# Optimization experiments

Hardware: AMD Instinct MI355X
Metric: run time of the kernel (lower is better)

Reference implementation:

```python
import jax, jax.numpy as jnp
import numpy as np
from math import sqrt

D = 64
HEADS = 8
SEQ = 4096


def setup_inputs() -> dict:
    key = jax.random.key(0)
    ks = jax.random.split(key, 11)
    d, h = D, HEADS
    scale = 1.0 / sqrt(d)
    inp = {
        "q": jax.random.normal(ks[0], (SEQ, d), dtype=jnp.float32),
        "k": jax.random.normal(ks[1], (SEQ, d), dtype=jnp.float32),
        "v": jax.random.normal(ks[2], (SEQ, d), dtype=jnp.float32),
        # Linear(d, d*heads) weights stored as [in, out]; biases [out]
        "qw_w": jax.random.normal(ks[3], (d, d * h), dtype=jnp.float32) * scale,
        "qw_b": jax.random.normal(ks[4], (d * h,), dtype=jnp.float32) * 0.01,
        "kw_w": jax.random.normal(ks[5], (d, d * h), dtype=jnp.float32) * scale,
        "kw_b": jax.random.normal(ks[6], (d * h,), dtype=jnp.float32) * 0.01,
        "vw_w": jax.random.normal(ks[7], (d, d * h), dtype=jnp.float32) * scale,
        "vw_b": jax.random.normal(ks[8], (d * h,), dtype=jnp.float32) * 0.01,
        "ow_w": jax.random.normal(ks[9], (d * h, d), dtype=jnp.float32) * (1.0 / sqrt(d * h)),
        "ow_b": jax.random.normal(ks[10], (d,), dtype=jnp.float32) * 0.01,
    }
    return inp


def reference(q, k, v, qw_w, qw_b, kw_w, kw_b, vw_w, vw_b, ow_w, ow_b):
    d, h = D, HEADS
    # Project: [S, d] @ [d, d*h] -> [S, d*h], then raw reshape to [h, S, d]
    # (matches torch .view(heads, -1, d) on the contiguous projection)
    qh = (q @ qw_w + qw_b).reshape(h, -1, d)
    kh = (k @ kw_w + kw_b).reshape(h, -1, d)
    vh = (v @ vw_w + vw_b).reshape(h, -1, d)
    # scores: [h, S, S]
    scores = jnp.einsum("hqd,hkd->hqk", qh, kh) / sqrt(d)
    attn = jax.nn.softmax(scores, axis=-1)
    ctx = jnp.einsum("hqk,hkd->hqd", attn, vh)  # [h, S, d]
    ctx = ctx.reshape(-1, h * d)  # row-major reshape, matches torch .reshape
    return ctx @ ow_w + ow_b  # [S, d]
```

## Files before the change

### kernel.cpp

```cpp
#include <hip/hip_runtime.h>
#include <stdint.h>

#define SEQL 4096
#define NHEAD 8
#define DHEAD 64
#define HEADELEMS (SEQL * DHEAD)
#define KVBLK 64
#define TPH 32

typedef unsigned short u16;
typedef __bf16 bf16x8 __attribute__((ext_vector_type(8)));
typedef float f32x16 __attribute__((ext_vector_type(16)));

extern "C" __device__ float __ocml_native_exp2_f32(float);

__device__ __forceinline__ u16 f2bf(float f) {
  union { float f; uint32_t u; } x; x.f = f;
  uint32_t r = x.u + 0x7fffu + ((x.u >> 16) & 1u);
  return (u16)(r >> 16);
}

__device__ __forceinline__ uint32_t cvt_pk_bf16(float lo, float hi) {
  uint32_t r;
  asm("v_cvt_pk_bf16_f32 %0, %1, %2" : "=v"(r) : "v"(lo), "v"(hi));
  return r;
}

__device__ __forceinline__ void pl32_swap(uint32_t& dst, uint32_t& src) {
  asm("v_permlane32_swap_b32 %0, %1" : "+v"(dst), "+v"(src));
}

#define GLDS16(g, l)                                                            \
  __builtin_amdgcn_global_load_lds(                                             \
      (const __attribute__((address_space(1))) uint32_t*)(g),                   \
      (__attribute__((address_space(3))) uint32_t*)(l), 16, 0, 0)

__global__ __launch_bounds__(256) void proj_kernel(
    const float* __restrict__ q, const float* __restrict__ k, const float* __restrict__ v,
    const float* __restrict__ qw, const float* __restrict__ qb,
    const float* __restrict__ kw, const float* __restrict__ kb,
    const float* __restrict__ vw, const float* __restrict__ vb,
    u16* __restrict__ Qp, u16* __restrict__ Kp, u16* __restrict__ vhT) {
  const float* X; const float* W; const float* B; float scale;
  if (blockIdx.y == 0)      { X = q; W = qw; B = qb; scale = 0.125f * 1.44269504089f; }
  else if (blockIdx.y == 1) { X = k; W = kw; B = kb; scale = 1.0f; }
  else                      { X = v; W = vw; B = vb; scale = 1.0f; }

  __shared__ float xs[16][64];
  __shared__ __align__(16) u16 vtile[64][136];
  const int t = threadIdx.x;
  const int rowbase = blockIdx.x * 16;
  for (int i = t; i < 16 * 64; i += 256) xs[i >> 6][i & 63] = X[rowbase * 64 + i];
  __syncthreads();

  const int c0 = t * 2;
  float acc0[16] = {}, acc1[16] = {};
  for (int kk = 0; kk < 64; ++kk) {
    const float2 w = *(const float2*)(W + kk * 512 + c0);
    #pragma unroll
    for (int r = 0; r < 16; ++r) {
      const float x = xs[r][kk];
      acc0[r] = fmaf(x, w.x, acc0[r]);
      acc1[r] = fmaf(x, w.y, acc1[r]);
    }
  }
  const float b0 = B[c0], b1 = B[c0 + 1];

  if (blockIdx.y != 2) {
    u16* __restrict__ P = (blockIdx.y == 0) ? Qp : Kp;
    #pragma unroll
    for (int r = 0; r < 16; ++r) {
      const u16 o0 = f2bf((acc0[r] + b0) * scale);
      const u16 o1 = f2bf((acc1[r] + b1) * scale);
      *(uint32_t*)(P + (rowbase + r) * 512 + c0) = ((uint32_t)o1 << 16) | (uint32_t)o0;
    }
  } else {
    const int dd = c0 & 63, cg = c0 >> 6;
    #pragma unroll
    for (int r = 0; r < 16; ++r) {
      vtile[dd][r * 8 + cg]     = f2bf(acc0[r] + b0);
      vtile[dd + 1][r * 8 + cg] = f2bf(acc1[r] + b1);
    }
    __syncthreads();
    const int h = rowbase >> 9;
    const int ibase = (rowbase & 511) * 8;
    u16* __restrict__ dst = vhT + h * HEADELEMS;
    #pragma unroll
    for (int rep = 0; rep < 4; ++rep) {
      const int n = t + rep * 256;
      const int d2 = n >> 4, m = n & 15;
      *(uint4*)(dst + d2 * 4096 + ibase + m * 8) = *(const uint4*)(&vtile[d2][m * 8]);
    }
  }
}

__global__ __launch_bounds__(256, 2) void attn_kernel(
    const u16* __restrict__ Qp, const u16* __restrict__ Kp,
    const u16* __restrict__ vhT, float* __restrict__ cxp, float* __restrict__ lsp) {
  const int h = blockIdx.x & 7, idx = blockIdx.x >> 3;
  const int qb = idx >> 1, half = idx & 1;
  const int t = threadIdx.x, lane = t & 63;
  const int l32 = lane & 31, hi = lane >> 5;

  __shared__ __align__(16) char smem[5 * 16384];

  const u16* __restrict__ Qh = Qp + h * HEADELEMS;
  const u16* __restrict__ Kh = Kp + h * HEADELEMS;
  const u16* __restrict__ VTh = vhT + h * HEADELEMS;

  int koff[2], voff[2];
  #pragma unroll
  for (int i = 0; i < 2; ++i) {
    const int n = t + i * 256;
    const int r = n >> 3, c = (n & 7) ^ (r & 7);
    koff[i] = r * 64 + c * 8;
    voff[i] = r * 4096 + c * 8;
  }
  const int wuni = (t & 192) * 16;
  char* const qlds = smem + 65536;

#define STAGE(j, slot)                                                         \
  {                                                                            \
    const int kb_ = (half * TPH + (j)) * KVBLK;                                \
    GLDS16(Kh + kb_ * 64 + koff[0], (slot));                                   \
    GLDS16(Kh + kb_ * 64 + koff[1], (slot) + 4096);                            \
    GLDS16(VTh + kb_ + voff[0], (slot) + 8192);                                \
    GLDS16(VTh + kb_ + voff[1], (slot) + 12288);                               \
  }

  {
    const u16* __restrict__ qsrc = Qh + qb * 128 * 64;
    #pragma unroll
    for (int i = 0; i < 4; ++i) {
      const int n = t + i * 256;
      GLDS16(qsrc + (n >> 3) * 64 + (n & 7) * 8, qlds + i * 4096 + wuni);
    }
  }
  __builtin_amdgcn_sched_barrier(0);
  STAGE(0, smem + wuni);
  __builtin_amdgcn_sched_barrier(0);
  STAGE(1, smem + 16384 + wuni);
  __builtin_amdgcn_sched_barrier(0);
  STAGE(2, smem + 32768 + wuni);
  __builtin_amdgcn_sched_barrier(0);

  asm volatile("s_waitcnt vmcnt(12)" ::: "memory");
  __builtin_amdgcn_s_barrier();
  __builtin_amdgcn_sched_barrier(0);

  const int qrl = (t >> 6) * 32 + l32;
  bf16x8 qf[4];
  #pragma unroll
  for (int ks = 0; ks < 4; ++ks)
    qf[ks] = *(const bf16x8*)(qlds + qrl * 128 + ks * 32 + hi * 16);

  const f32x16 z16 = {0,0,0,0,0,0,0,0,0,0,0,0,0,0,0,0};
  f32x16 ca0 = z16, ca1 = z16;
  float ls[4] = {0.f, 0.f, 0.f, 0.f};

  for (int it = 0; it < TPH; ++it) {
    if (it < TPH - 2)       asm volatile("s_waitcnt vmcnt(8) lgkmcnt(0)" ::: "memory");
    else if (it == TPH - 2) asm volatile("s_waitcnt vmcnt(4) lgkmcnt(0)" ::: "memory");
    else                    asm volatile("s_waitcnt vmcnt(0) lgkmcnt(0)" ::: "memory");
    __builtin_amdgcn_s_barrier();
    __builtin_amdgcn_sched_barrier(0);

    char* const cb = smem + (it & 3) * 16384;
    if (it + 3 < TPH) STAGE(it + 3, smem + ((it + 3) & 3) * 16384 + wuni);
    __builtin_amdgcn_sched_barrier(0);

    f32x16 s0 = z16, s1 = z16;
    const int ar0 = l32, ar1 = l32 + 32;
    __builtin_amdgcn_s_setprio(1);
    #pragma unroll
    for (int ks = 0; ks < 4; ++ks) {
      const int c = ks * 2 + hi;
      const bf16x8 k0 = *(const bf16x8*)(cb + ar0 * 128 + ((c ^ (ar0 & 7)) * 16));
      const bf16x8 k1 = *(const bf16x8*)(cb + ar1 * 128 + ((c ^ (ar1 & 7)) * 16));
      s0 = __builtin_amdgcn_mfma_f32_32x32x16_bf16(k0, qf[ks], s0, 0, 0, 0);
      s1 = __builtin_amdgcn_mfma_f32_32x32x16_bf16(k1, qf[ks], s1, 0, 0, 0);
    }
    __builtin_amdgcn_s_setprio(0);

    float e[32];
    #pragma unroll
    for (int r = 0; r < 16; ++r) { e[r] = __ocml_native_exp2_f32(s0[r]); ls[r & 3] += e[r]; }
    #pragma unroll
    for (int r = 0; r < 16; ++r) { e[16 + r] = __ocml_native_exp2_f32(s1[r]); ls[r & 3] += e[16 + r]; }

    #pragma unroll
    for (int ksl = 0; ksl < 4; ++ksl) {
      uint32_t w0 = cvt_pk_bf16(e[ksl * 8 + 0], e[ksl * 8 + 1]);
      uint32_t w1 = cvt_pk_bf16(e[ksl * 8 + 2], e[ksl * 8 + 3]);
      uint32_t w2 = cvt_pk_bf16(e[ksl * 8 + 4], e[ksl * 8 + 5]);
      uint32_t w3 = cvt_pk_bf16(e[ksl * 8 + 6], e[ksl * 8 + 7]);
      pl32_swap(w0, w2);
      pl32_swap(w1, w3);
      union { uint32_t u[4]; bf16x8 v; } pw;
      pw.u[0] = w0; pw.u[1] = w1; pw.u[2] = w2; pw.u[3] = w3;
      const bf16x8 paf = pw.v;

      const int cl = ksl * 2 + hi;
      const int vr0 = l32, vr1 = l32 + 32;
      const bf16x8 v0 = *(const bf16x8*)(cb + 8192 + vr0 * 128 + ((cl ^ (vr0 & 7)) * 16));
      const bf16x8 v1 = *(const bf16x8*)(cb + 8192 + vr1 * 128 + ((cl ^ (vr1 & 7)) * 16));
      __builtin_amdgcn_s_setprio(1);
      ca0 = __builtin_amdgcn_mfma_f32_32x32x16_bf16(paf, v0, ca0, 0, 0, 0);
      ca1 = __builtin_amdgcn_mfma_f32_32x32x16_bf16(paf, v1, ca1, 0, 0, 0);
      __builtin_amdgcn_s_setprio(0);
    }
  }
#undef STAGE

  float lsum = (ls[0] + ls[1]) + (ls[2] + ls[3]);
  lsum += __shfl_xor(lsum, 32);
  const int q0 = qb * 128 + (t >> 6) * 32;
  float* __restrict__ ch = cxp + (half * NHEAD + h) * HEADELEMS;
  #pragma unroll
  for (int reg = 0; reg < 16; ++reg) {
    const int crw = (reg & 3) + 8 * (reg >> 2) + 4 * hi;
    ch[(q0 + crw) * 64 + l32]      = ca0[reg];
    ch[(q0 + crw) * 64 + 32 + l32] = ca1[reg];
  }
  if (hi == 0) lsp[(half * NHEAD + h) * SEQL + q0 + l32] = lsum;
}

__global__ __launch_bounds__(256) void outproj_kernel(
    const float* __restrict__ cxp, const float* __restrict__ lsp,
    const float* __restrict__ W, const float* __restrict__ B,
    float* __restrict__ out) {
  const int t = threadIdx.x;
  const int r0 = blockIdx.x * 8;
  const int hh = r0 >> 9;
  const int sb0 = (r0 & 511) * 8;

  __shared__ float cn[64][64];
  __shared__ float invs[64];

  if (t < 64)
    invs[t] = 1.0f / (lsp[hh * SEQL + sb0 + t] + lsp[(NHEAD + hh) * SEQL + sb0 + t]);
  __syncthreads();

  const float* __restrict__ a0 = cxp + hh * HEADELEMS + sb0 * 64;
  const float* __restrict__ b0 = cxp + (NHEAD + hh) * HEADELEMS + sb0 * 64;
  #pragma unroll
  for (int i = 0; i < 4; ++i) {
    const int n = (t + i * 256) * 4;
    const int s = n >> 6;
    const float4 av = *(const float4*)(a0 + n);
    const float4 bv = *(const float4*)(b0 + n);
    const float inv = invs[s];
    float4 cv;
    cv.x = (av.x + bv.x) * inv; cv.y = (av.y + bv.y) * inv;
    cv.z = (av.z + bv.z) * inv; cv.w = (av.w + bv.w) * inv;
    *(float4*)(&cn[s][n & 63]) = cv;
  }
  __syncthreads();

  const int col = t & 63;
  const int lr = (t >> 6) * 2;
  float acc0 = 0.f, acc1 = 0.f;
  #pragma unroll 8
  for (int kk = 0; kk < 512; ++kk) {
    const float wv = W[kk * 64 + col];
    acc0 = fmaf(cn[lr * 8 + (kk >> 6)][kk & 63], wv, acc0);
    acc1 = fmaf(cn[lr * 8 + 8 + (kk >> 6)][kk & 63], wv, acc1);
  }
  const float b = B[col];
  out[(r0 + lr) * 64 + col] = acc0 + b;
  out[(r0 + lr + 1) * 64 + col] = acc1 + b;
}

extern "C" void kernel_launch(void* const* d_in, const int* in_sizes, int n_in,
                              void* d_out, int out_size, void* d_ws, size_t ws_size,
                              hipStream_t stream) {
  const float* q  = (const float*)d_in[0];
  const float* k  = (const float*)d_in[1];
  const float* v  = (const float*)d_in[2];
  const float* qw = (const float*)d_in[3];
  const float* qb = (const float*)d_in[4];
  const float* kw = (const float*)d_in[5];
  const float* kb = (const float*)d_in[6];
  const float* vw = (const float*)d_in[7];
  const float* vb = (const float*)d_in[8];
  const float* ow = (const float*)d_in[9];
  const float* ob = (const float*)d_in[10];

  char* ws = (char*)d_ws;
  u16* Qp    = (u16*)(ws);
  u16* Kp    = (u16*)(ws + (4u << 20));
  u16* vhT   = (u16*)(ws + (8u << 20));
  float* cxp = (float*)(ws + (12u << 20));
  float* lsp = (float*)(ws + (28u << 20));
  float* out = (float*)d_out;

  proj_kernel<<<dim3(SEQL / 16, 3), 256, 0, stream>>>(q, k, v, qw, qb, kw, kb, vw, vb,
                                                      Qp, Kp, vhT);
  attn_kernel<<<512, 256, 0, stream>>>(Qp, Kp, vhT, cxp, lsp);
  outproj_kernel<<<SEQL / 8, 256, 0, stream>>>(cxp, lsp, ow, ob, out);
}
```

Before: 91.67 us.

## Double Q rows per attention block and split KV four ways

Each attention block now handles 256 query rows, two 32-row Q fragments per wave, so every K/V tile loaded into LDS feeds twice as many MFMAs. To keep the grid at 512 blocks, the KV range is split into 4 parts (SPLIT template) instead of 2. The LDS pipeline shrinks from 4 stages to 3 to make room for the larger Q tile. The out-projection sums the 4 partial contexts and row sums, which adds global traffic and register pressure, and falls back to SPLIT=2 if the workspace is too small.

```diff
diff --git a/kernel.cpp b/kernel.cpp
--- a/kernel.cpp
+++ b/kernel.cpp
@@ -6,7 +6,6 @@
 #define DHEAD 64
 #define HEADELEMS (SEQL * DHEAD)
 #define KVBLK 64
-#define TPH 32
 
 typedef unsigned short u16;
 typedef __bf16 bf16x8 __attribute__((ext_vector_type(8)));
@@ -28,6 +27,18 @@
 
 __device__ __forceinline__ void pl32_swap(uint32_t& dst, uint32_t& src) {
   asm("v_permlane32_swap_b32 %0, %1" : "+v"(dst), "+v"(src));
+}
+
+__device__ __forceinline__ bf16x8 pack_paf(const float* e8) {
+  uint32_t w0 = cvt_pk_bf16(e8[0], e8[1]);
+  uint32_t w1 = cvt_pk_bf16(e8[2], e8[3]);
+  uint32_t w2 = cvt_pk_bf16(e8[4], e8[5]);
+  uint32_t w3 = cvt_pk_bf16(e8[6], e8[7]);
+  pl32_swap(w0, w2);
+  pl32_swap(w1, w3);
+  union { uint32_t u[4]; bf16x8 v; } pw;
+  pw.u[0] = w0; pw.u[1] = w1; pw.u[2] = w2; pw.u[3] = w3;
+  return pw.v;
 }
 
 #define GLDS16(g, l)                                                            \
@@ -94,15 +105,18 @@
   }
 }
 
+template <int SPLIT>
 __global__ __launch_bounds__(256, 2) void attn_kernel(
     const u16* __restrict__ Qp, const u16* __restrict__ Kp,
     const u16* __restrict__ vhT, float* __restrict__ cxp, float* __restrict__ lsp) {
+  constexpr int TPQ = 64 / SPLIT;
   const int h = blockIdx.x & 7, idx = blockIdx.x >> 3;
-  const int qb = idx >> 1, half = idx & 1;
+  const int qb = idx / SPLIT, part = idx % SPLIT;
   const int t = threadIdx.x, lane = t & 63;
   const int l32 = lane & 31, hi = lane >> 5;
 
-  __shared__ __align__(16) char smem[5 * 16384];
+  __shared__ __align__(16) char smem[3 * 16384 + 32768];
+  char* const qlds = smem + 49152;
 
   const u16* __restrict__ Qh = Qp + h * HEADELEMS;
   const u16* __restrict__ Kh = Kp + h * HEADELEMS;
@@ -117,11 +131,10 @@
     voff[i] = r * 4096 + c * 8;
   }
   const int wuni = (t & 192) * 16;
-  char* const qlds = smem + 65536;
 
 #define STAGE(j, slot)                                                         \
   {                                                                            \
-    const int kb_ = (half * TPH + (j)) * KVBLK;                                \
+    const int kb_ = (part * TPQ + (j)) * KVBLK;                                \
     GLDS16(Kh + kb_ * 64 + koff[0], (slot));                                   \
     GLDS16(Kh + kb_ * 64 + koff[1], (slot) + 4096);                            \
     GLDS16(VTh + kb_ + voff[0], (slot) + 8192);                                \
@@ -129,9 +142,9 @@
   }
 
   {
-    const u16* __restrict__ qsrc = Qh + qb * 128 * 64;
-    #pragma unroll
-    for (int i = 0; i < 4; ++i) {
+    const u16* __restrict__ qsrc = Qh + qb * 256 * 64;
+    #pragma unroll
+    for (int i = 0; i < 8; ++i) {
       const int n = t + i * 256;
       GLDS16(qsrc + (n >> 3) * 64 + (n & 7) * 8, qlds + i * 4096 + wuni);
     }
@@ -141,35 +154,34 @@
   __builtin_amdgcn_sched_barrier(0);
   STAGE(1, smem + 16384 + wuni);
   __builtin_amdgcn_sched_barrier(0);
-  STAGE(2, smem + 32768 + wuni);
-  __builtin_amdgcn_sched_barrier(0);
-
-  asm volatile("s_waitcnt vmcnt(12)" ::: "memory");
+
+  asm volatile("s_waitcnt vmcnt(8)" ::: "memory");
   __builtin_amdgcn_s_barrier();
   __builtin_amdgcn_sched_barrier(0);
 
-  const int qrl = (t >> 6) * 32 + l32;
-  bf16x8 qf[4];
+  const int qrlA = (t >> 6) * 64 + l32;
+  bf16x8 qfA[4], qfB[4];
   #pragma unroll
-  for (int ks = 0; ks < 4; ++ks)
-    qf[ks] = *(const bf16x8*)(qlds + qrl * 128 + ks * 32 + hi * 16);
+  for (int ks = 0; ks < 4; ++ks) {
+    qfA[ks] = *(const bf16x8*)(qlds + qrlA * 128 + ks * 32 + hi * 16);
+    qfB[ks] = *(const bf16x8*)(qlds + (qrlA + 32) * 128 + ks * 32 + hi * 16);
+  }
 
   const f32x16 z16 = {0,0,0,0,0,0,0,0,0,0,0,0,0,0,0,0};
-  f32x16 ca0 = z16, ca1 = z16;
-  float ls[4] = {0.f, 0.f, 0.f, 0.f};
-
-  for (int it = 0; it < TPH; ++it) {
-    if (it < TPH - 2)       asm volatile("s_waitcnt vmcnt(8) lgkmcnt(0)" ::: "memory");
-    else if (it == TPH - 2) asm volatile("s_waitcnt vmcnt(4) lgkmcnt(0)" ::: "memory");
-    else                    asm volatile("s_waitcnt vmcnt(0) lgkmcnt(0)" ::: "memory");
+  f32x16 caA0 = z16, caA1 = z16, caB0 = z16, caB1 = z16;
+  float lsA[4] = {0.f, 0.f, 0.f, 0.f}, lsB[4] = {0.f, 0.f, 0.f, 0.f};
+
+  for (int it = 0; it < TPQ; ++it) {
+    if (it < TPQ - 1) asm volatile("s_waitcnt vmcnt(4) lgkmcnt(0)" ::: "memory");
+    else              asm volatile("s_waitcnt vmcnt(0) lgkmcnt(0)" ::: "memory");
     __builtin_amdgcn_s_barrier();
     __builtin_amdgcn_sched_barrier(0);
 
-    char* const cb = smem + (it & 3) * 16384;
-    if (it + 3 < TPH) STAGE(it + 3, smem + ((it + 3) & 3) * 16384 + wuni);
+    char* const cb = smem + (it % 3) * 16384;
+    if (it + 2 < TPQ) STAGE(it + 2, smem + ((it + 2) % 3) * 16384 + wuni);
     __builtin_amdgcn_sched_barrier(0);
 
-    f32x16 s0 = z16, s1 = z16;
+    f32x16 sA0 = z16, sA1 = z16, sB0 = z16, sB1 = z16;
     const int ar0 = l32, ar1 = l32 + 32;
     __builtin_amdgcn_s_setprio(1);
     #pragma unroll
@@ -177,54 +189,70 @@
       const int c = ks * 2 + hi;
       const bf16x8 k0 = *(const bf16x8*)(cb + ar0 * 128 + ((c ^ (ar0 & 7)) * 16));
       const bf16x8 k1 = *(const bf16x8*)(cb + ar1 * 128 + ((c ^ (ar1 & 7)) * 16));
-      s0 = __builtin_amdgcn_mfma_f32_32x32x16_bf16(k0, qf[ks], s0, 0, 0, 0);
-      s1 = __builtin_amdgcn_mfma_f32_32x32x16_bf16(k1, qf[ks], s1, 0, 0, 0);
+      sA0 = __builtin_amdgcn_mfma_f32_32x32x16_bf16(k0, qfA[ks], sA0, 0, 0, 0);
+      sA1 = __builtin_amdgcn_mfma_f32_32x32x16_bf16(k1, qfA[ks], sA1, 0, 0, 0);
+      sB0 = __builtin_amdgcn_mfma_f32_32x32x16_bf16(k0, qfB[ks], sB0, 0, 0, 0);
+      sB1 = __builtin_amdgcn_mfma_f32_32x32x16_bf16(k1, qfB[ks], sB1, 0, 0, 0);
     }
     __builtin_amdgcn_s_setprio(0);
 
-    float e[32];
-    #pragma unroll
-    for (int r = 0; r < 16; ++r) { e[r] = __ocml_native_exp2_f32(s0[r]); ls[r & 3] += e[r]; }
-    #pragma unroll
-    for (int r = 0; r < 16; ++r) { e[16 + r] = __ocml_native_exp2_f32(s1[r]); ls[r & 3] += e[16 + r]; }
+    bf16x8 pafA[4], pafB[4];
+    {
+      float e[32];
+      #pragma unroll
+      for (int r = 0; r < 16; ++r) { e[r] = __ocml_native_exp2_f32(sA0[r]); lsA[r & 3] += e[r]; }
+      #pragma unroll
+      for (int r = 0; r < 16; ++r) { e[16 + r] = __ocml_native_exp2_f32(sA1[r]); lsA[r & 3] += e[16 + r]; }
+      #pragma unroll
+      for (int ksl = 0; ksl < 4; ++ksl) pafA[ksl] = pack_paf(e + ksl * 8);
+    }
+    {
+      float e[32];
+      #pragma unroll
+      for (int r = 0; r < 16; ++r) { e[r] = __ocml_native_exp2_f32(sB0[r]); lsB[r & 3] += e[r]; }
+      #pragma unroll
+      for (int r = 0; r < 16; ++r) { e[16 + r] = __ocml_native_exp2_f32(sB1[r]); lsB[r & 3] += e[16 + r]; }
+      #pragma unroll
+      for (int ksl = 0; ksl < 4; ++ksl) pafB[ksl] = pack_paf(e + ksl * 8);
+    }
 
     #pragma unroll
     for (int ksl = 0; ksl < 4; ++ksl) {
-      uint32_t w0 = cvt_pk_bf16(e[ksl * 8 + 0], e[ksl * 8 + 1]);
-      uint32_t w1 = cvt_pk_bf16(e[ksl * 8 + 2], e[ksl * 8 + 3]);
-      uint32_t w2 = cvt_pk_bf16(e[ksl * 8 + 4], e[ksl * 8 + 5]);
-      uint32_t w3 = cvt_pk_bf16(e[ksl * 8 + 6], e[ksl * 8 + 7]);
-      pl32_swap(w0, w2);
-      pl32_swap(w1, w3);
-      union { uint32_t u[4]; bf16x8 v; } pw;
-      pw.u[0] = w0; pw.u[1] = w1; pw.u[2] = w2; pw.u[3] = w3;
-      const bf16x8 paf = pw.v;
-
       const int cl = ksl * 2 + hi;
       const int vr0 = l32, vr1 = l32 + 32;
       const bf16x8 v0 = *(const bf16x8*)(cb + 8192 + vr0 * 128 + ((cl ^ (vr0 & 7)) * 16));
       const bf16x8 v1 = *(const bf16x8*)(cb + 8192 + vr1 * 128 + ((cl ^ (vr1 & 7)) * 16));
       __builtin_amdgcn_s_setprio(1);
-      ca0 = __builtin_amdgcn_mfma_f32_32x32x16_bf16(paf, v0, ca0, 0, 0, 0);
-      ca1 = __builtin_amdgcn_mfma_f32_32x32x16_bf16(paf, v1, ca1, 0, 0, 0);
+      caA0 = __builtin_amdgcn_mfma_f32_32x32x16_bf16(pafA[ksl], v0, caA0, 0, 0, 0);
+      caA1 = __builtin_amdgcn_mfma_f32_32x32x16_bf16(pafA[ksl], v1, caA1, 0, 0, 0);
+      caB0 = __builtin_amdgcn_mfma_f32_32x32x16_bf16(pafB[ksl], v0, caB0, 0, 0, 0);
+      caB1 = __builtin_amdgcn_mfma_f32_32x32x16_bf16(pafB[ksl], v1, caB1, 0, 0, 0);
       __builtin_amdgcn_s_setprio(0);
     }
   }
 #undef STAGE
 
-  float lsum = (ls[0] + ls[1]) + (ls[2] + ls[3]);
-  lsum += __shfl_xor(lsum, 32);
-  const int q0 = qb * 128 + (t >> 6) * 32;
-  float* __restrict__ ch = cxp + (half * NHEAD + h) * HEADELEMS;
+  float lsumA = (lsA[0] + lsA[1]) + (lsA[2] + lsA[3]);
+  float lsumB = (lsB[0] + lsB[1]) + (lsB[2] + lsB[3]);
+  lsumA += __shfl_xor(lsumA, 32);
+  lsumB += __shfl_xor(lsumB, 32);
+  const int q0 = qb * 256 + (t >> 6) * 64;
+  float* __restrict__ ch = cxp + (part * NHEAD + h) * HEADELEMS;
   #pragma unroll
   for (int reg = 0; reg < 16; ++reg) {
     const int crw = (reg & 3) + 8 * (reg >> 2) + 4 * hi;
-    ch[(q0 + crw) * 64 + l32]      = ca0[reg];
-    ch[(q0 + crw) * 64 + 32 + l32] = ca1[reg];
-  }
-  if (hi == 0) lsp[(half * NHEAD + h) * SEQL + q0 + l32] = lsum;
-}
-
+    ch[(q0 + crw) * 64 + l32]           = caA0[reg];
+    ch[(q0 + crw) * 64 + 32 + l32]      = caA1[reg];
+    ch[(q0 + 32 + crw) * 64 + l32]      = caB0[reg];
+    ch[(q0 + 32 + crw) * 64 + 32 + l32] = caB1[reg];
+  }
+  if (hi == 0) {
+    lsp[(part * NHEAD + h) * SEQL + q0 + l32]      = lsumA;
+    lsp[(part * NHEAD + h) * SEQL + q0 + 32 + l32] = lsumB;
+  }
+}
+
+template <int SPLIT>
 __global__ __launch_bounds__(256) void outproj_kernel(
     const float* __restrict__ cxp, const float* __restrict__ lsp,
     const float* __restrict__ W, const float* __restrict__ B,
@@ -237,23 +265,28 @@
   __shared__ float cn[64][64];
   __shared__ float invs[64];
 
-  if (t < 64)
-    invs[t] = 1.0f / (lsp[hh * SEQL + sb0 + t] + lsp[(NHEAD + hh) * SEQL + sb0 + t]);
+  if (t < 64) {
+    float s = 0.f;
+    #pragma unroll
+    for (int p = 0; p < SPLIT; ++p) s += lsp[(p * NHEAD + hh) * SEQL + sb0 + t];
+    invs[t] = 1.0f / s;
+  }
   __syncthreads();
 
-  const float* __restrict__ a0 = cxp + hh * HEADELEMS + sb0 * 64;
-  const float* __restrict__ b0 = cxp + (NHEAD + hh) * HEADELEMS + sb0 * 64;
   #pragma unroll
   for (int i = 0; i < 4; ++i) {
     const int n = (t + i * 256) * 4;
     const int s = n >> 6;
-    const float4 av = *(const float4*)(a0 + n);
-    const float4 bv = *(const float4*)(b0 + n);
+    const int base = hh * HEADELEMS + sb0 * 64 + n;
+    float4 av = *(const float4*)(cxp + base);
+    #pragma unroll
+    for (int p = 1; p < SPLIT; ++p) {
+      const float4 bv = *(const float4*)(cxp + p * NHEAD * HEADELEMS + base);
+      av.x += bv.x; av.y += bv.y; av.z += bv.z; av.w += bv.w;
+    }
     const float inv = invs[s];
-    float4 cv;
-    cv.x = (av.x + bv.x) * inv; cv.y = (av.y + bv.y) * inv;
-    cv.z = (av.z + bv.z) * inv; cv.w = (av.w + bv.w) * inv;
-    *(float4*)(&cn[s][n & 63]) = cv;
+    av.x *= inv; av.y *= inv; av.z *= inv; av.w *= inv;
+    *(float4*)(&cn[s][n & 63]) = av;
   }
   __syncthreads();
 
@@ -291,11 +324,19 @@
   u16* Kp    = (u16*)(ws + (4u << 20));
   u16* vhT   = (u16*)(ws + (8u << 20));
   float* cxp = (float*)(ws + (12u << 20));
-  float* lsp = (float*)(ws + (28u << 20));
   float* out = (float*)d_out;
 
   proj_kernel<<<dim3(SEQL / 16, 3), 256, 0, stream>>>(q, k, v, qw, qb, kw, kb, vw, vb,
                                                       Qp, Kp, vhT);
-  attn_kernel<<<512, 256, 0, stream>>>(Qp, Kp, vhT, cxp, lsp);
-  outproj_kernel<<<SEQL / 8, 256, 0, stream>>>(cxp, lsp, ow, ob, out);
-}
+
+  const size_t need4 = (12u << 20) + 4u * ((8u << 20) + NHEAD * SEQL * 4u);
+  if (ws_size >= need4) {
+    float* lsp = (float*)(ws + (12u << 20) + 4u * (8u << 20));
+    attn_kernel<4><<<16 * 4 * 8, 256, 0, stream>>>(Qp, Kp, vhT, cxp, lsp);
+    outproj_kernel<4><<<SEQL / 8, 256, 0, stream>>>(cxp, lsp, ow, ob, out);
+  } else {
+    float* lsp = (float*)(ws + (12u << 20) + 2u * (8u << 20));
+    attn_kernel<2><<<16 * 2 * 8, 256, 0, stream>>>(Qp, Kp, vhT, cxp, lsp);
+    outproj_kernel<2><<<SEQL / 8, 256, 0, stream>>>(cxp, lsp, ow, ob, out);
+  }
+}
```

Measured after the change: 89.21 us (median of 4 runs). -2.7%, faster.

## Split attention KV range three ways with smaller LDS and higher occupancy

Applied to the files above, without the earlier changes.

Templates the attention kernel on a KV split factor and launches a 3-way split (768 blocks) when workspace allows, falling back to 2. LDS drops from 80KB to 48KB by using a 3-slot ring with prefetch distance 2 and loading Q fragments directly from global instead of staging through LDS. Launch bounds raise to 3 waves/SIMD group for occupancy. The output projection sums SPLIT partial contexts and row sums, which adds partial-buffer traffic, and the shallower prefetch depth may expose more load latency.

```diff
diff --git a/kernel.cpp b/kernel.cpp
--- a/kernel.cpp
+++ b/kernel.cpp
@@ -6,7 +6,6 @@
 #define DHEAD 64
 #define HEADELEMS (SEQL * DHEAD)
 #define KVBLK 64
-#define TPH 32
 
 typedef unsigned short u16;
 typedef __bf16 bf16x8 __attribute__((ext_vector_type(8)));
@@ -28,6 +27,18 @@
 
 __device__ __forceinline__ void pl32_swap(uint32_t& dst, uint32_t& src) {
   asm("v_permlane32_swap_b32 %0, %1" : "+v"(dst), "+v"(src));
+}
+
+__device__ __forceinline__ bf16x8 pack_paf(const float* e8) {
+  uint32_t w0 = cvt_pk_bf16(e8[0], e8[1]);
+  uint32_t w1 = cvt_pk_bf16(e8[2], e8[3]);
+  uint32_t w2 = cvt_pk_bf16(e8[4], e8[5]);
+  uint32_t w3 = cvt_pk_bf16(e8[6], e8[7]);
+  pl32_swap(w0, w2);
+  pl32_swap(w1, w3);
+  union { uint32_t u[4]; bf16x8 v; } pw;
+  pw.u[0] = w0; pw.u[1] = w1; pw.u[2] = w2; pw.u[3] = w3;
+  return pw.v;
 }
 
 #define GLDS16(g, l)                                                            \
@@ -94,15 +105,18 @@
   }
 }
 
-__global__ __launch_bounds__(256, 2) void attn_kernel(
+template <int SPLIT>
+__global__ __launch_bounds__(256, 3) void attn_kernel(
     const u16* __restrict__ Qp, const u16* __restrict__ Kp,
     const u16* __restrict__ vhT, float* __restrict__ cxp, float* __restrict__ lsp) {
   const int h = blockIdx.x & 7, idx = blockIdx.x >> 3;
-  const int qb = idx >> 1, half = idx & 1;
+  const int qb = idx / SPLIT, part = idx % SPLIT;
   const int t = threadIdx.x, lane = t & 63;
   const int l32 = lane & 31, hi = lane >> 5;
-
-  __shared__ __align__(16) char smem[5 * 16384];
+  const int ts = (part * 64) / SPLIT;
+  const int te = ((part + 1) * 64) / SPLIT;
+
+  __shared__ __align__(16) char smem[3 * 16384];
 
   const u16* __restrict__ Qh = Qp + h * HEADELEMS;
   const u16* __restrict__ Kh = Kp + h * HEADELEMS;
@@ -117,56 +131,40 @@
     voff[i] = r * 4096 + c * 8;
   }
   const int wuni = (t & 192) * 16;
-  char* const qlds = smem + 65536;
 
 #define STAGE(j, slot)                                                         \
   {                                                                            \
-    const int kb_ = (half * TPH + (j)) * KVBLK;                                \
+    const int kb_ = (j) * KVBLK;                                               \
     GLDS16(Kh + kb_ * 64 + koff[0], (slot));                                   \
     GLDS16(Kh + kb_ * 64 + koff[1], (slot) + 4096);                            \
     GLDS16(VTh + kb_ + voff[0], (slot) + 8192);                                \
     GLDS16(VTh + kb_ + voff[1], (slot) + 12288);                               \
   }
 
-  {
-    const u16* __restrict__ qsrc = Qh + qb * 128 * 64;
-    #pragma unroll
-    for (int i = 0; i < 4; ++i) {
-      const int n = t + i * 256;
-      GLDS16(qsrc + (n >> 3) * 64 + (n & 7) * 8, qlds + i * 4096 + wuni);
-    }
-  }
-  __builtin_amdgcn_sched_barrier(0);
-  STAGE(0, smem + wuni);
-  __builtin_amdgcn_sched_barrier(0);
-  STAGE(1, smem + 16384 + wuni);
-  __builtin_amdgcn_sched_barrier(0);
-  STAGE(2, smem + 32768 + wuni);
-  __builtin_amdgcn_sched_barrier(0);
-
-  asm volatile("s_waitcnt vmcnt(12)" ::: "memory");
-  __builtin_amdgcn_s_barrier();
-  __builtin_amdgcn_sched_barrier(0);
-
-  const int qrl = (t >> 6) * 32 + l32;
+  const int qrow = qb * 128 + (t >> 6) * 32 + l32;
   bf16x8 qf[4];
   #pragma unroll
   for (int ks = 0; ks < 4; ++ks)
-    qf[ks] = *(const bf16x8*)(qlds + qrl * 128 + ks * 32 + hi * 16);
+    qf[ks] = *(const bf16x8*)(Qh + qrow * 64 + ks * 16 + hi * 8);
+  __builtin_amdgcn_sched_barrier(0);
+
+  STAGE(ts, smem + wuni);
+  __builtin_amdgcn_sched_barrier(0);
+  STAGE(ts + 1, smem + 16384 + wuni);
+  __builtin_amdgcn_sched_barrier(0);
 
   const f32x16 z16 = {0,0,0,0,0,0,0,0,0,0,0,0,0,0,0,0};
   f32x16 ca0 = z16, ca1 = z16;
   float ls[4] = {0.f, 0.f, 0.f, 0.f};
 
-  for (int it = 0; it < TPH; ++it) {
-    if (it < TPH - 2)       asm volatile("s_waitcnt vmcnt(8) lgkmcnt(0)" ::: "memory");
-    else if (it == TPH - 2) asm volatile("s_waitcnt vmcnt(4) lgkmcnt(0)" ::: "memory");
-    else                    asm volatile("s_waitcnt vmcnt(0) lgkmcnt(0)" ::: "memory");
+  for (int it = ts; it < te; ++it) {
+    if (it < te - 1) asm volatile("s_waitcnt vmcnt(4) lgkmcnt(0)" ::: "memory");
+    else             asm volatile("s_waitcnt vmcnt(0) lgkmcnt(0)" ::: "memory");
     __builtin_amdgcn_s_barrier();
     __builtin_amdgcn_sched_barrier(0);
 
-    char* const cb = smem + (it & 3) * 16384;
-    if (it + 3 < TPH) STAGE(it + 3, smem + ((it + 3) & 3) * 16384 + wuni);
+    char* const cb = smem + ((it - ts) % 3) * 16384;
+    if (it + 2 < te) STAGE(it + 2, smem + ((it - ts + 2) % 3) * 16384 + wuni);
     __builtin_amdgcn_sched_barrier(0);
 
     f32x16 s0 = z16, s1 = z16;
@@ -190,16 +188,7 @@
 
     #pragma unroll
     for (int ksl = 0; ksl < 4; ++ksl) {
-      uint32_t w0 = cvt_pk_bf16(e[ksl * 8 + 0], e[ksl * 8 + 1]);
-      uint32_t w1 = cvt_pk_bf16(e[ksl * 8 + 2], e[ksl * 8 + 3]);
-      uint32_t w2 = cvt_pk_bf16(e[ksl * 8 + 4], e[ksl * 8 + 5]);
-      uint32_t w3 = cvt_pk_bf16(e[ksl * 8 + 6], e[ksl * 8 + 7]);
-      pl32_swap(w0, w2);
-      pl32_swap(w1, w3);
-      union { uint32_t u[4]; bf16x8 v; } pw;
-      pw.u[0] = w0; pw.u[1] = w1; pw.u[2] = w2; pw.u[3] = w3;
-      const bf16x8 paf = pw.v;
-
+      const bf16x8 paf = pack_paf(e + ksl * 8);
       const int cl = ksl * 2 + hi;
       const int vr0 = l32, vr1 = l32 + 32;
       const bf16x8 v0 = *(const bf16x8*)(cb + 8192 + vr0 * 128 + ((cl ^ (vr0 & 7)) * 16));
@@ -215,16 +204,17 @@
   float lsum = (ls[0] + ls[1]) + (ls[2] + ls[3]);
   lsum += __shfl_xor(lsum, 32);
   const int q0 = qb * 128 + (t >> 6) * 32;
-  float* __restrict__ ch = cxp + (half * NHEAD + h) * HEADELEMS;
+  float* __restrict__ ch = cxp + (part * NHEAD + h) * HEADELEMS;
   #pragma unroll
   for (int reg = 0; reg < 16; ++reg) {
     const int crw = (reg & 3) + 8 * (reg >> 2) + 4 * hi;
     ch[(q0 + crw) * 64 + l32]      = ca0[reg];
     ch[(q0 + crw) * 64 + 32 + l32] = ca1[reg];
   }
-  if (hi == 0) lsp[(half * NHEAD + h) * SEQL + q0 + l32] = lsum;
-}
-
+  if (hi == 0) lsp[(part * NHEAD + h) * SEQL + q0 + l32] = lsum;
+}
+
+template <int SPLIT>
 __global__ __launch_bounds__(256) void outproj_kernel(
     const float* __restrict__ cxp, const float* __restrict__ lsp,
     const float* __restrict__ W, const float* __restrict__ B,
@@ -237,23 +227,28 @@
   __shared__ float cn[64][64];
   __shared__ float invs[64];
 
-  if (t < 64)
-    invs[t] = 1.0f / (lsp[hh * SEQL + sb0 + t] + lsp[(NHEAD + hh) * SEQL + sb0 + t]);
+  if (t < 64) {
+    float s = 0.f;
+    #pragma unroll
+    for (int p = 0; p < SPLIT; ++p) s += lsp[(p * NHEAD + hh) * SEQL + sb0 + t];
+    invs[t] = 1.0f / s;
+  }
   __syncthreads();
 
-  const float* __restrict__ a0 = cxp + hh * HEADELEMS + sb0 * 64;
-  const float* __restrict__ b0 = cxp + (NHEAD + hh) * HEADELEMS + sb0 * 64;
   #pragma unroll
   for (int i = 0; i < 4; ++i) {
     const int n = (t + i * 256) * 4;
     const int s = n >> 6;
-    const float4 av = *(const float4*)(a0 + n);
-    const float4 bv = *(const float4*)(b0 + n);
+    const int base = hh * HEADELEMS + sb0 * 64 + n;
+    float4 av = *(const float4*)(cxp + base);
+    #pragma unroll
+    for (int p = 1; p < SPLIT; ++p) {
+      const float4 bv = *(const float4*)(cxp + p * NHEAD * HEADELEMS + base);
+      av.x += bv.x; av.y += bv.y; av.z += bv.z; av.w += bv.w;
+    }
     const float inv = invs[s];
-    float4 cv;
-    cv.x = (av.x + bv.x) * inv; cv.y = (av.y + bv.y) * inv;
-    cv.z = (av.z + bv.z) * inv; cv.w = (av.w + bv.w) * inv;
-    *(float4*)(&cn[s][n & 63]) = cv;
+    av.x *= inv; av.y *= inv; av.z *= inv; av.w *= inv;
+    *(float4*)(&cn[s][n & 63]) = av;
   }
   __syncthreads();
 
@@ -291,11 +286,19 @@
   u16* Kp    = (u16*)(ws + (4u << 20));
   u16* vhT   = (u16*)(ws + (8u << 20));
   float* cxp = (float*)(ws + (12u << 20));
-  float* lsp = (float*)(ws + (28u << 20));
   float* out = (float*)d_out;
 
   proj_kernel<<<dim3(SEQL / 16, 3), 256, 0, stream>>>(q, k, v, qw, qb, kw, kb, vw, vb,
                                                       Qp, Kp, vhT);
-  attn_kernel<<<512, 256, 0, stream>>>(Qp, Kp, vhT, cxp, lsp);
-  outproj_kernel<<<SEQL / 8, 256, 0, stream>>>(cxp, lsp, ow, ob, out);
-}
+
+  const size_t need3 = (12u << 20) + 3u * ((8u << 20) + NHEAD * SEQL * 4u);
+  if (ws_size >= need3) {
+    float* lsp = (float*)(ws + (12u << 20) + 3u * (8u << 20));
+    attn_kernel<3><<<32 * 3 * 8, 256, 0, stream>>>(Qp, Kp, vhT, cxp, lsp);
+    outproj_kernel<3><<<SEQL / 8, 256, 0, stream>>>(cxp, lsp, ow, ob, out);
+  } else {
+    float* lsp = (float*)(ws + (12u << 20) + 2u * (8u << 20));
+    attn_kernel<2><<<32 * 2 * 8, 256, 0, stream>>>(Qp, Kp, vhT, cxp, lsp);
+    outproj_kernel<2><<<SEQL / 8, 256, 0, stream>>>(cxp, lsp, ow, ob, out);
+  }
+}
```

After: 90.25 us. About the same (-1.5%).
